# Kernel tuning notes

Hardware: AMD Instinct MI355X
Metric: run time of the kernel (lower is better)

The kernel has to match this reference:

```python
import jax, jax.numpy as jnp
import numpy as np

BATCH_SIZE = 2048
N_PARENTS = 256
N_FEATURES = 32
N_GLOBAL = 16
N_BRANCHES = 4
OFFSET = 262144  # nodes from levels before the parent level


def reshape_features(mtx, n_parents, batch_size, n_branches, n_features):
    # Redistribute [n_parents*batch, n_branches*n_features] -> [n_parents*n_branches*batch, n_features]
    # preserving node>event>branch ordering, exactly as the torch.jit.script helper.
    m = mtx.reshape(n_parents, batch_size, n_features * n_branches)
    m = jnp.swapaxes(m, 1, 2)
    m = m.reshape(n_parents * n_branches, n_features, batch_size)
    m = jnp.swapaxes(m, 1, 2)
    return m.reshape(n_parents * n_branches * batch_size, n_features)


def setup_inputs() -> dict:
    key = jax.random.key(0)
    k = jax.random.split(key, 5)
    n_rows = OFFSET + N_PARENTS * BATCH_SIZE
    x = jax.random.normal(k[0], (n_rows, N_FEATURES), dtype=jnp.float32)
    global_features = jax.random.normal(k[1], (BATCH_SIZE, N_GLOBAL), dtype=jnp.float32)
    # parent nodes occupy contiguous rows [OFFSET, OFFSET + n_parents*batch)
    parents_idxs = jnp.arange(N_PARENTS * BATCH_SIZE, dtype=jnp.int32) + OFFSET
    d_in = N_FEATURES + N_GLOBAL
    d_out = N_FEATURES * N_BRANCHES
    W1 = jax.random.normal(k[2], (d_in, d_out), dtype=jnp.float32) * 0.05
    b1 = jnp.zeros((d_out,), dtype=jnp.float32)
    W2 = jax.random.normal(k[3], (d_out, d_out), dtype=jnp.float32) * 0.05
    b2 = jnp.zeros((d_out,), dtype=jnp.float32)
    return {"x": x, "global_features": global_features, "parents_idxs": parents_idxs,
            "W1": W1, "b1": b1, "W2": W2, "b2": b2}


def reference(x, global_features, parents_idxs, W1, b1, W2, b2):
    # Gather parent node features and per-event global features
    parents_ftxs = x[parents_idxs]                                   # [P*B, F]
    parent_global = global_features[parents_idxs % BATCH_SIZE]      # [P*B, G]
    h = jnp.concatenate([parents_ftxs, parent_global], axis=-1)     # [P*B, F+G]
    # proj_nn: small MLP (Linear -> LeakyReLU -> Linear), torch LeakyReLU default slope 0.01
    h = jax.nn.leaky_relu(h @ W1 + b1, negative_slope=0.01)
    proj_ftx = h @ W2 + b2                                           # [P*B, BR*F]
    # residual: repeat_interleave each feature n_branches times along feature dim
    proj_ftx = proj_ftx + jnp.repeat(parents_ftxs, N_BRANCHES, axis=-1)
    children_ftxs = reshape_features(proj_ftx, N_PARENTS, BATCH_SIZE, N_BRANCHES, N_FEATURES)
    return jnp.concatenate([x, children_ftxs], axis=0)
```

## Files before the change

kernel.cpp:

```cpp
#include <hip/hip_runtime.h>

#define BATCH   2048
#define NPAR    256
#define NF      32
#define NG      16
#define NBR     4
#define OFS     262144
#define DOUT    128
#define NROWSX  (OFS + NPAR*BATCH)
#define MROWS   (NPAR*BATCH)
#define NTILES  (MROWS/16)
#define CHBASE  (NROWSX*NF)
#define NMLP    4096
#define NCOPY   2048

typedef short bf16x8 __attribute__((ext_vector_type(8)));
typedef float f32x4  __attribute__((ext_vector_type(4)));

#define WSOFF_W2F  1048576
#define WSOFF_W1F  (1048576 + 32768)

__device__ __forceinline__ unsigned short f2bf(float f){
  unsigned int u = __float_as_uint(f);
  u += 0x7FFFu + ((u >> 16) & 1u);
  return (unsigned short)(u >> 16);
}

__global__ void k_g1(const float* __restrict__ gf, const float* __restrict__ W1,
                     const float* __restrict__ b1, const float* __restrict__ W2,
                     char* __restrict__ ws){
  int bid = blockIdx.x, tid = threadIdx.x;
  if (bid < 1024){
    int idx = bid*256 + tid;
    int e = idx >> 7, j = idx & 127;
    float s = b1[j];
    const float* grow = gf + e*NG;
    const float* w = W1 + NF*DOUT + j;
    #pragma unroll
    for (int k = 0; k < NG; k++) s = fmaf(grow[k], w[k*DOUT], s);
    ((float*)ws)[idx] = s;
    return;
  }
  int t = (bid - 1024)*256 + tid;
  if (t < 2048){
    int f = t >> 6, l = t & 63;
    int kk = f >> 3, n = f & 7;
    int krow = 32*kk + 8*(l >> 4);
    int col  = 16*n + (l & 15);
    union { uint4 q; unsigned short u[8]; } w;
    #pragma unroll
    for (int e = 0; e < 8; e++) w.u[e] = f2bf(W2[(krow + e)*DOUT + col]);
    ((uint4*)(ws + WSOFF_W2F))[t] = w.q;
  } else {
    int q = t - 2048;
    int n = q >> 6, l = q & 63;
    int kb = 8*(l >> 4);
    int col = 16*n + (l & 15);
    union { uint4 v; unsigned short u[8]; } w;
    #pragma unroll
    for (int e = 0; e < 8; e++) w.u[e] = f2bf(W1[(kb + e)*DOUT + col]);
    ((uint4*)(ws + WSOFF_W1F))[q] = w.v;
  }
}

__global__ __launch_bounds__(512, 4) void k_main(
    const float* __restrict__ x, const int* __restrict__ pidx,
    const float* __restrict__ b2, const char* __restrict__ ws,
    float* __restrict__ out)
{
  __shared__ uint4 sB2[2048];
  __shared__ uint4 sW1[512];
  __shared__ uint4 sH1[2048];

  const int bid = blockIdx.x;
  const int tid = threadIdx.x;

  if (bid % 3 == 2){
    const int cid = bid / 3;
    const int n = NROWSX*NF/4;
    const float4* src4 = (const float4*)x;
    float4* dst4 = (float4*)out;
    for (int i = cid*512 + tid; i < n; i += NCOPY*512)
      dst4[i] = src4[i];
    return;
  }
  const int mid = (bid/3)*2 + (bid % 3);

  const uint4* W2f = (const uint4*)(ws + WSOFF_W2F);
  const uint4* W1f = (const uint4*)(ws + WSOFF_W1F);
  #pragma unroll
  for (int i = 0; i < 4; i++) sB2[i*512 + tid] = W2f[i*512 + tid];
  sW1[tid] = W1f[tid & 511];
  __syncthreads();

  const int lane = tid & 63;
  const int wv   = tid >> 6;
  const int r15  = lane & 15;
  const int g    = lane >> 4;
  const float* G1 = (const float*)ws;

  char* h1base = (char*)sH1 + wv*4096;
  const bf16x8* B2f = (const bf16x8*)sB2;
  const bf16x8* B1f = (const bf16x8*)sW1;

  const int tl   = mid*8 + wv;
  const int row0 = tl*16;

  const int idxA = pidx[row0 + r15];

  const float* ap = x + idxA*NF + 8*g;
  float4 a0 = *(const float4*)ap;
  float4 a1 = *(const float4*)(ap + 4);
  float xres[8];
  #pragma unroll
  for (int n = 0; n < 8; n++) xres[n] = x[idxA*NF + 4*n + g];

  union { bf16x8 v; unsigned short u[8]; } af;
  af.u[0]=f2bf(a0.x); af.u[1]=f2bf(a0.y); af.u[2]=f2bf(a0.z); af.u[3]=f2bf(a0.w);
  af.u[4]=f2bf(a1.x); af.u[5]=f2bf(a1.y); af.u[6]=f2bf(a1.z); af.u[7]=f2bf(a1.w);

  const int g1r = idxA & (BATCH-1);
  f32x4 acc1[8];
  #pragma unroll
  for (int n = 0; n < 8; n++)
    acc1[n] = *(const f32x4*)(G1 + g1r*DOUT + 16*n + 4*g);
  #pragma unroll
  for (int n = 0; n < 8; n++)
    acc1[n] = __builtin_amdgcn_mfma_f32_16x16x32_bf16(B1f[n*64 + lane], af.v, acc1[n], 0, 0, 0);

  #pragma unroll
  for (int n = 0; n < 8; n++){
    float v0 = acc1[n][0], v1 = acc1[n][1], v2 = acc1[n][2], v3 = acc1[n][3];
    v0 = v0 > 0.f ? v0 : 0.01f*v0;
    v1 = v1 > 0.f ? v1 : 0.01f*v1;
    v2 = v2 > 0.f ? v2 : 0.01f*v2;
    v3 = v3 > 0.f ? v3 : 0.01f*v3;
    uint2 pk;
    pk.x = (unsigned)f2bf(v0) | ((unsigned)f2bf(v1) << 16);
    pk.y = (unsigned)f2bf(v2) | ((unsigned)f2bf(v3) << 16);
    int off = r15*256 + (16*n + 4*g)*2;
    off ^= (r15 & 7) << 4;
    *(uint2*)(h1base + off) = pk;
  }

  f32x4 acc2[8];
  #pragma unroll
  for (int n = 0; n < 8; n++)
    acc2[n] = *(const f32x4*)(b2 + 16*n + 4*g);
  #pragma unroll
  for (int kk = 0; kk < 4; kk++){
    int roff = r15*256 + 64*kk + 16*g;
    roff ^= (r15 & 7) << 4;
    bf16x8 a2 = *(const bf16x8*)(h1base + roff);
    #pragma unroll
    for (int n = 0; n < 8; n++)
      acc2[n] = __builtin_amdgcn_mfma_f32_16x16x32_bf16(B2f[(kk*8 + n)*64 + lane], a2, acc2[n], 0, 0, 0);
  }

  const int p  = row0 >> 11;
  const int b0 = row0 & (BATCH-1);
  const int orow = CHBASE + ((p*NBR)*BATCH + b0 + r15)*NF;
  #pragma unroll
  for (int n = 0; n < 8; n++){
    int c0 = 16*n + 4*g;
    int br = c0 >> 5, fc0 = c0 & 31;
    f32x4 v = acc2[n];
    float rsd = xres[n];
    v[0] += rsd; v[1] += rsd; v[2] += rsd; v[3] += rsd;
    *(f32x4*)(out + orow + br*(BATCH*NF) + fc0) = v;
  }
}

extern "C" void kernel_launch(void* const* d_in, const int* in_sizes, int n_in,
                              void* d_out, int out_size, void* d_ws, size_t ws_size,
                              hipStream_t stream){
  const float* x   = (const float*)d_in[0];
  const float* gf  = (const float*)d_in[1];
  const int*   pidx= (const int*)d_in[2];
  const float* W1  = (const float*)d_in[3];
  const float* b1  = (const float*)d_in[4];
  const float* W2  = (const float*)d_in[5];
  const float* b2  = (const float*)d_in[6];
  float* out = (float*)d_out;
  char* ws   = (char*)d_ws;

  k_g1  <<<1034, 256, 0, stream>>>(gf, W1, b1, W2, ws);
  k_main<<<NMLP + NCOPY, 512, 0, stream>>>(x, pidx, b2, ws, out);
}
```

Before: 162.9 us.

## Fuse copy into MLP waves, process four tiles per wave with prefetch

```diff
diff --git a/kernel.cpp b/kernel.cpp
--- a/kernel.cpp
+++ b/kernel.cpp
@@ -1,4 +1,5 @@
 #include <hip/hip_runtime.h>
+#include <hip/hip_bf16.h>
 
 #define BATCH   2048
 #define NPAR    256
@@ -11,8 +12,8 @@
 #define MROWS   (NPAR*BATCH)
 #define NTILES  (MROWS/16)
 #define CHBASE  (NROWSX*NF)
-#define NMLP    4096
-#define NCOPY   2048
+#define NMLP    1024
+#define CPN4    (NROWSX*NF/4)
 
 typedef short bf16x8 __attribute__((ext_vector_type(8)));
 typedef float f32x4  __attribute__((ext_vector_type(4)));
@@ -75,22 +76,11 @@
   const int bid = blockIdx.x;
   const int tid = threadIdx.x;
 
-  if (bid % 3 == 2){
-    const int cid = bid / 3;
-    const int n = NROWSX*NF/4;
-    const float4* src4 = (const float4*)x;
-    float4* dst4 = (float4*)out;
-    for (int i = cid*512 + tid; i < n; i += NCOPY*512)
-      dst4[i] = src4[i];
-    return;
-  }
-  const int mid = (bid/3)*2 + (bid % 3);
-
   const uint4* W2f = (const uint4*)(ws + WSOFF_W2F);
   const uint4* W1f = (const uint4*)(ws + WSOFF_W1F);
   #pragma unroll
   for (int i = 0; i < 4; i++) sB2[i*512 + tid] = W2f[i*512 + tid];
-  sW1[tid] = W1f[tid & 511];
+  sW1[tid] = W1f[tid];
   __syncthreads();
 
   const int lane = tid & 63;
@@ -98,76 +88,117 @@
   const int r15  = lane & 15;
   const int g    = lane >> 4;
   const float* G1 = (const float*)ws;
+  const float4* src4 = (const float4*)x;
+  float4* dst4 = (float4*)out;
 
   char* h1base = (char*)sH1 + wv*4096;
   const bf16x8* B2f = (const bf16x8*)sB2;
   const bf16x8* B1f = (const bf16x8*)sW1;
 
-  const int tl   = mid*8 + wv;
-  const int row0 = tl*16;
-
-  const int idxA = pidx[row0 + r15];
-
-  const float* ap = x + idxA*NF + 8*g;
-  float4 a0 = *(const float4*)ap;
-  float4 a1 = *(const float4*)(ap + 4);
-  float xres[8];
+  const int w    = bid*8 + wv;
+  const int gtid = bid*512 + tid;
+
+  int idx4[4];
   #pragma unroll
-  for (int n = 0; n < 8; n++) xres[n] = x[idxA*NF + 4*n + g];
-
-  union { bf16x8 v; unsigned short u[8]; } af;
-  af.u[0]=f2bf(a0.x); af.u[1]=f2bf(a0.y); af.u[2]=f2bf(a0.z); af.u[3]=f2bf(a0.w);
-  af.u[4]=f2bf(a1.x); af.u[5]=f2bf(a1.y); af.u[6]=f2bf(a1.z); af.u[7]=f2bf(a1.w);
-
-  const int g1r = idxA & (BATCH-1);
-  f32x4 acc1[8];
+  for (int t = 0; t < 4; t++) idx4[t] = pidx[w*64 + t*16 + r15];
+
+  const float* ap0 = x + idx4[0]*NF + 8*g;
+  float4 a0 = *(const float4*)ap0;
+  float4 a1 = *(const float4*)(ap0 + 4);
+  f32x4 g1n[8];
+  {
+    const float* gp = G1 + (idx4[0] & (BATCH-1))*DOUT + 4*g;
+    #pragma unroll
+    for (int n = 0; n < 8; n++) g1n[n] = *(const f32x4*)(gp + 16*n);
+  }
+
   #pragma unroll
-  for (int n = 0; n < 8; n++)
-    acc1[n] = *(const f32x4*)(G1 + g1r*DOUT + 16*n + 4*g);
-  #pragma unroll
-  for (int n = 0; n < 8; n++)
-    acc1[n] = __builtin_amdgcn_mfma_f32_16x16x32_bf16(B1f[n*64 + lane], af.v, acc1[n], 0, 0, 0);
-
-  #pragma unroll
-  for (int n = 0; n < 8; n++){
-    float v0 = acc1[n][0], v1 = acc1[n][1], v2 = acc1[n][2], v3 = acc1[n][3];
-    v0 = v0 > 0.f ? v0 : 0.01f*v0;
-    v1 = v1 > 0.f ? v1 : 0.01f*v1;
-    v2 = v2 > 0.f ? v2 : 0.01f*v2;
-    v3 = v3 > 0.f ? v3 : 0.01f*v3;
-    uint2 pk;
-    pk.x = (unsigned)f2bf(v0) | ((unsigned)f2bf(v1) << 16);
-    pk.y = (unsigned)f2bf(v2) | ((unsigned)f2bf(v3) << 16);
-    int off = r15*256 + (16*n + 4*g)*2;
-    off ^= (r15 & 7) << 4;
-    *(uint2*)(h1base + off) = pk;
-  }
-
-  f32x4 acc2[8];
-  #pragma unroll
-  for (int n = 0; n < 8; n++)
-    acc2[n] = *(const f32x4*)(b2 + 16*n + 4*g);
-  #pragma unroll
-  for (int kk = 0; kk < 4; kk++){
-    int roff = r15*256 + 64*kk + 16*g;
-    roff ^= (r15 & 7) << 4;
-    bf16x8 a2 = *(const bf16x8*)(h1base + roff);
+  for (int t = 0; t < 4; t++){
+    const int row0 = w*64 + t*16;
+    const int idxA = idx4[t];
+
+    float4 cp0 = src4[(t*3+0)*(NMLP*512) + gtid];
+    float4 cp1 = src4[(t*3+1)*(NMLP*512) + gtid];
+    float4 cp2 = src4[(t*3+2)*(NMLP*512) + gtid];
+
+    union { bf16x8 v; __hip_bfloat162 h[4]; } af;
+    af.h[0] = __float22bfloat162_rn(make_float2(a0.x, a0.y));
+    af.h[1] = __float22bfloat162_rn(make_float2(a0.z, a0.w));
+    af.h[2] = __float22bfloat162_rn(make_float2(a1.x, a1.y));
+    af.h[3] = __float22bfloat162_rn(make_float2(a1.z, a1.w));
+
+    f32x4 acc1[8];
+    #pragma unroll
+    for (int n = 0; n < 8; n++) acc1[n] = g1n[n];
+
+    float4 a0n = a0, a1n = a1;
+    if (t < 3){
+      const float* apn = x + idx4[t+1]*NF + 8*g;
+      a0n = *(const float4*)apn;
+      a1n = *(const float4*)(apn + 4);
+    }
+
     #pragma unroll
     for (int n = 0; n < 8; n++)
-      acc2[n] = __builtin_amdgcn_mfma_f32_16x16x32_bf16(B2f[(kk*8 + n)*64 + lane], a2, acc2[n], 0, 0, 0);
-  }
-
-  const int p  = row0 >> 11;
-  const int b0 = row0 & (BATCH-1);
-  const int orow = CHBASE + ((p*NBR)*BATCH + b0 + r15)*NF;
-  #pragma unroll
-  for (int n = 0; n < 8; n++){
-    int c0 = 16*n + 4*g;
-    int br = c0 >> 5, fc0 = c0 & 31;
-    f32x4 v = acc2[n];
-    float rsd = xres[n];
-    v[0] += rsd; v[1] += rsd; v[2] += rsd; v[3] += rsd;
-    *(f32x4*)(out + orow + br*(BATCH*NF) + fc0) = v;
+      acc1[n] = __builtin_amdgcn_mfma_f32_16x16x32_bf16(B1f[n*64 + lane], af.v, acc1[n], 0, 0, 0);
+
+    #pragma unroll
+    for (int n = 0; n < 8; n++){
+      float v0 = acc1[n][0], v1 = acc1[n][1], v2 = acc1[n][2], v3 = acc1[n][3];
+      v0 = v0 > 0.f ? v0 : 0.01f*v0;
+      v1 = v1 > 0.f ? v1 : 0.01f*v1;
+      v2 = v2 > 0.f ? v2 : 0.01f*v2;
+      v3 = v3 > 0.f ? v3 : 0.01f*v3;
+      union { uint2 q; __hip_bfloat162 h[2]; } pk;
+      pk.h[0] = __float22bfloat162_rn(make_float2(v0, v1));
+      pk.h[1] = __float22bfloat162_rn(make_float2(v2, v3));
+      int off = r15*256 + (16*n + 4*g)*2;
+      off ^= (r15 & 7) << 4;
+      *(uint2*)(h1base + off) = pk.q;
+    }
+
+    if (t < 3){
+      const float* gp = G1 + (idx4[t+1] & (BATCH-1))*DOUT + 4*g;
+      #pragma unroll
+      for (int n = 0; n < 8; n++) g1n[n] = *(const f32x4*)(gp + 16*n);
+    }
+
+    float xres[8];
+    #pragma unroll
+    for (int n = 0; n < 8; n++) xres[n] = x[idxA*NF + 4*n + g];
+
+    f32x4 acc2[8];
+    #pragma unroll
+    for (int n = 0; n < 8; n++)
+      acc2[n] = *(const f32x4*)(b2 + 16*n + 4*g);
+    #pragma unroll
+    for (int kk = 0; kk < 4; kk++){
+      int roff = r15*256 + 64*kk + 16*g;
+      roff ^= (r15 & 7) << 4;
+      bf16x8 a2 = *(const bf16x8*)(h1base + roff);
+      #pragma unroll
+      for (int n = 0; n < 8; n++)
+        acc2[n] = __builtin_amdgcn_mfma_f32_16x16x32_bf16(B2f[(kk*8 + n)*64 + lane], a2, acc2[n], 0, 0, 0);
+    }
+
+    const int p  = row0 >> 11;
+    const int b0 = row0 & (BATCH-1);
+    const int orow = CHBASE + ((p*NBR)*BATCH + b0 + r15)*NF;
+    #pragma unroll
+    for (int n = 0; n < 8; n++){
+      int c0 = 16*n + 4*g;
+      int br = c0 >> 5, fc0 = c0 & 31;
+      f32x4 v = acc2[n];
+      float rsd = xres[n];
+      v[0] += rsd; v[1] += rsd; v[2] += rsd; v[3] += rsd;
+      *(f32x4*)(out + orow + br*(BATCH*NF) + fc0) = v;
+    }
+
+    dst4[(t*3+0)*(NMLP*512) + gtid] = cp0;
+    dst4[(t*3+1)*(NMLP*512) + gtid] = cp1;
+    dst4[(t*3+2)*(NMLP*512) + gtid] = cp2;
+
+    a0 = a0n; a1 = a1n;
   }
 }
 
@@ -185,5 +216,5 @@
   char* ws   = (char*)d_ws;
 
   k_g1  <<<1034, 256, 0, stream>>>(gf, W1, b1, W2, ws);
-  k_main<<<NMLP + NCOPY, 512, 0, stream>>>(x, pidx, b2, ws, out);
-}
+  k_main<<<NMLP, 512, 0, stream>>>(x, pidx, b2, ws, out);
+}
```

Measured after the change: 197.8 us. 21.4% more time.

## Loop four tiles per wave with prefetch and fold residual into MFMA

Applied to the files above, without the earlier changes.

```diff
diff --git a/kernel.cpp b/kernel.cpp
--- a/kernel.cpp
+++ b/kernel.cpp
@@ -1,4 +1,5 @@
 #include <hip/hip_runtime.h>
+#include <hip/hip_bf16.h>
 
 #define BATCH   2048
 #define NPAR    256
@@ -9,16 +10,17 @@
 #define DOUT    128
 #define NROWSX  (OFS + NPAR*BATCH)
 #define MROWS   (NPAR*BATCH)
-#define NTILES  (MROWS/16)
 #define CHBASE  (NROWSX*NF)
-#define NMLP    4096
+#define NMLP    1024
 #define NCOPY   2048
+#define CPN4    (NROWSX*NF/4)
 
 typedef short bf16x8 __attribute__((ext_vector_type(8)));
 typedef float f32x4  __attribute__((ext_vector_type(4)));
 
 #define WSOFF_W2F  1048576
 #define WSOFF_W1F  (1048576 + 32768)
+#define WSOFF_RF   (1048576 + 32768 + 8192)
 
 __device__ __forceinline__ unsigned short f2bf(float f){
   unsigned int u = __float_as_uint(f);
@@ -26,9 +28,9 @@
   return (unsigned short)(u >> 16);
 }
 
-__global__ void k_g1(const float* __restrict__ gf, const float* __restrict__ W1,
-                     const float* __restrict__ b1, const float* __restrict__ W2,
-                     char* __restrict__ ws){
+__global__ void k_prep(const float* __restrict__ gf, const float* __restrict__ W1,
+                       const float* __restrict__ b1, const float* __restrict__ W2,
+                       char* __restrict__ ws){
   int bid = blockIdx.x, tid = threadIdx.x;
   if (bid < 1024){
     int idx = bid*256 + tid;
@@ -51,7 +53,7 @@
     #pragma unroll
     for (int e = 0; e < 8; e++) w.u[e] = f2bf(W2[(krow + e)*DOUT + col]);
     ((uint4*)(ws + WSOFF_W2F))[t] = w.q;
-  } else {
+  } else if (t < 2560){
     int q = t - 2048;
     int n = q >> 6, l = q & 63;
     int kb = 8*(l >> 4);
@@ -60,6 +62,15 @@
     #pragma unroll
     for (int e = 0; e < 8; e++) w.u[e] = f2bf(W1[(kb + e)*DOUT + col]);
     ((uint4*)(ws + WSOFF_W1F))[q] = w.v;
+  } else {
+    int q = t - 2560;
+    int n = q >> 6, l = q & 63;
+    int g = l >> 4, r = l & 15;
+    int e1 = 4*n + (r >> 2) - 8*g;
+    union { uint4 v; unsigned short u[8]; } w;
+    #pragma unroll
+    for (int e = 0; e < 8; e++) w.u[e] = (e == e1) ? 0x3F80 : 0;
+    ((uint4*)(ws + WSOFF_RF))[q] = w.v;
   }
 }
 
@@ -69,28 +80,28 @@
     float* __restrict__ out)
 {
   __shared__ uint4 sB2[2048];
-  __shared__ uint4 sW1[512];
+  __shared__ uint4 sWR[1024];
   __shared__ uint4 sH1[2048];
 
   const int bid = blockIdx.x;
   const int tid = threadIdx.x;
 
-  if (bid % 3 == 2){
-    const int cid = bid / 3;
-    const int n = NROWSX*NF/4;
+  if (bid % 3){
+    const int cid = (bid/3)*2 + (bid % 3) - 1;
     const float4* src4 = (const float4*)x;
     float4* dst4 = (float4*)out;
-    for (int i = cid*512 + tid; i < n; i += NCOPY*512)
+    for (int i = cid*512 + tid; i < CPN4; i += NCOPY*512)
       dst4[i] = src4[i];
     return;
   }
-  const int mid = (bid/3)*2 + (bid % 3);
+  const int mid = bid/3;
 
   const uint4* W2f = (const uint4*)(ws + WSOFF_W2F);
-  const uint4* W1f = (const uint4*)(ws + WSOFF_W1F);
+  const uint4* WRf = (const uint4*)(ws + WSOFF_W1F);
   #pragma unroll
   for (int i = 0; i < 4; i++) sB2[i*512 + tid] = W2f[i*512 + tid];
-  sW1[tid] = W1f[tid & 511];
+  sWR[tid] = WRf[tid];
+  sWR[512 + tid] = WRf[512 + tid];
   __syncthreads();
 
   const int lane = tid & 63;
@@ -101,73 +112,85 @@
 
   char* h1base = (char*)sH1 + wv*4096;
   const bf16x8* B2f = (const bf16x8*)sB2;
-  const bf16x8* B1f = (const bf16x8*)sW1;
-
-  const int tl   = mid*8 + wv;
-  const int row0 = tl*16;
-
-  const int idxA = pidx[row0 + r15];
-
+  const bf16x8* B1f = (const bf16x8*)sWR;
+  const bf16x8* Rf  = (const bf16x8*)(sWR + 512);
+
+  const int w = mid*8 + wv;
+
+  int idxA = pidx[w*64 + r15];
   const float* ap = x + idxA*NF + 8*g;
   float4 a0 = *(const float4*)ap;
   float4 a1 = *(const float4*)(ap + 4);
-  float xres[8];
-  #pragma unroll
-  for (int n = 0; n < 8; n++) xres[n] = x[idxA*NF + 4*n + g];
-
-  union { bf16x8 v; unsigned short u[8]; } af;
-  af.u[0]=f2bf(a0.x); af.u[1]=f2bf(a0.y); af.u[2]=f2bf(a0.z); af.u[3]=f2bf(a0.w);
-  af.u[4]=f2bf(a1.x); af.u[5]=f2bf(a1.y); af.u[6]=f2bf(a1.z); af.u[7]=f2bf(a1.w);
-
-  const int g1r = idxA & (BATCH-1);
-  f32x4 acc1[8];
-  #pragma unroll
-  for (int n = 0; n < 8; n++)
-    acc1[n] = *(const f32x4*)(G1 + g1r*DOUT + 16*n + 4*g);
-  #pragma unroll
-  for (int n = 0; n < 8; n++)
-    acc1[n] = __builtin_amdgcn_mfma_f32_16x16x32_bf16(B1f[n*64 + lane], af.v, acc1[n], 0, 0, 0);
-
-  #pragma unroll
-  for (int n = 0; n < 8; n++){
-    float v0 = acc1[n][0], v1 = acc1[n][1], v2 = acc1[n][2], v3 = acc1[n][3];
-    v0 = v0 > 0.f ? v0 : 0.01f*v0;
-    v1 = v1 > 0.f ? v1 : 0.01f*v1;
-    v2 = v2 > 0.f ? v2 : 0.01f*v2;
-    v3 = v3 > 0.f ? v3 : 0.01f*v3;
-    uint2 pk;
-    pk.x = (unsigned)f2bf(v0) | ((unsigned)f2bf(v1) << 16);
-    pk.y = (unsigned)f2bf(v2) | ((unsigned)f2bf(v3) << 16);
-    int off = r15*256 + (16*n + 4*g)*2;
-    off ^= (r15 & 7) << 4;
-    *(uint2*)(h1base + off) = pk;
-  }
-
-  f32x4 acc2[8];
-  #pragma unroll
-  for (int n = 0; n < 8; n++)
-    acc2[n] = *(const f32x4*)(b2 + 16*n + 4*g);
-  #pragma unroll
-  for (int kk = 0; kk < 4; kk++){
-    int roff = r15*256 + 64*kk + 16*g;
-    roff ^= (r15 & 7) << 4;
-    bf16x8 a2 = *(const bf16x8*)(h1base + roff);
-    #pragma unroll
-    for (int n = 0; n < 8; n++)
-      acc2[n] = __builtin_amdgcn_mfma_f32_16x16x32_bf16(B2f[(kk*8 + n)*64 + lane], a2, acc2[n], 0, 0, 0);
-  }
-
-  const int p  = row0 >> 11;
-  const int b0 = row0 & (BATCH-1);
-  const int orow = CHBASE + ((p*NBR)*BATCH + b0 + r15)*NF;
-  #pragma unroll
-  for (int n = 0; n < 8; n++){
-    int c0 = 16*n + 4*g;
-    int br = c0 >> 5, fc0 = c0 & 31;
-    f32x4 v = acc2[n];
-    float rsd = xres[n];
-    v[0] += rsd; v[1] += rsd; v[2] += rsd; v[3] += rsd;
-    *(f32x4*)(out + orow + br*(BATCH*NF) + fc0) = v;
+
+  for (int t = 0; t < 4; t++){
+    const int row0 = w*64 + t*16;
+
+    const int tn = (t < 3) ? t+1 : 3;
+    const int idxn = pidx[w*64 + tn*16 + r15];
+
+    const int g1r = idxA & (BATCH-1);
+    f32x4 acc1[8];
+    #pragma unroll
+    for (int n = 0; n < 8; n++)
+      acc1[n] = *(const f32x4*)(G1 + g1r*DOUT + 16*n + 4*g);
+
+    union { bf16x8 v; __hip_bfloat162 h[4]; } af;
+    af.h[0] = __float22bfloat162_rn(make_float2(a0.x, a0.y));
+    af.h[1] = __float22bfloat162_rn(make_float2(a0.z, a0.w));
+    af.h[2] = __float22bfloat162_rn(make_float2(a1.x, a1.y));
+    af.h[3] = __float22bfloat162_rn(make_float2(a1.z, a1.w));
+
+    #pragma unroll
+    for (int n = 0; n < 8; n++)
+      acc1[n] = __builtin_amdgcn_mfma_f32_16x16x32_bf16(B1f[n*64 + lane], af.v, acc1[n], 0, 0, 0);
+
+    const float* apn = x + idxn*NF + 8*g;
+    float4 a0n = *(const float4*)apn;
+    float4 a1n = *(const float4*)(apn + 4);
+
+    #pragma unroll
+    for (int n = 0; n < 8; n++){
+      float v0 = acc1[n][0], v1 = acc1[n][1], v2 = acc1[n][2], v3 = acc1[n][3];
+      v0 = v0 > 0.f ? v0 : 0.01f*v0;
+      v1 = v1 > 0.f ? v1 : 0.01f*v1;
+      v2 = v2 > 0.f ? v2 : 0.01f*v2;
+      v3 = v3 > 0.f ? v3 : 0.01f*v3;
+      union { uint2 q; __hip_bfloat162 h[2]; } pk;
+      pk.h[0] = __float22bfloat162_rn(make_float2(v0, v1));
+      pk.h[1] = __float22bfloat162_rn(make_float2(v2, v3));
+      int off = r15*256 + (16*n + 4*g)*2;
+      off ^= (r15 & 7) << 4;
+      *(uint2*)(h1base + off) = pk.q;
+    }
+
+    f32x4 acc2[8];
+    #pragma unroll
+    for (int n = 0; n < 8; n++)
+      acc2[n] = *(const f32x4*)(b2 + 16*n + 4*g);
+    #pragma unroll
+    for (int n = 0; n < 8; n++)
+      acc2[n] = __builtin_amdgcn_mfma_f32_16x16x32_bf16(Rf[n*64 + lane], af.v, acc2[n], 0, 0, 0);
+    #pragma unroll
+    for (int kk = 0; kk < 4; kk++){
+      int roff = r15*256 + 64*kk + 16*g;
+      roff ^= (r15 & 7) << 4;
+      bf16x8 a2 = *(const bf16x8*)(h1base + roff);
+      #pragma unroll
+      for (int n = 0; n < 8; n++)
+        acc2[n] = __builtin_amdgcn_mfma_f32_16x16x32_bf16(B2f[(kk*8 + n)*64 + lane], a2, acc2[n], 0, 0, 0);
+    }
+
+    const int p  = row0 >> 11;
+    const int b0 = row0 & (BATCH-1);
+    const int orow = CHBASE + ((p*NBR)*BATCH + b0 + r15)*NF;
+    #pragma unroll
+    for (int n = 0; n < 8; n++){
+      int c0 = 16*n + 4*g;
+      int br = c0 >> 5, fc0 = c0 & 31;
+      *(f32x4*)(out + orow + br*(BATCH*NF) + fc0) = acc2[n];
+    }
+
+    idxA = idxn; a0 = a0n; a1 = a1n;
   }
 }
 
@@ -184,6 +207,6 @@
   float* out = (float*)d_out;
   char* ws   = (char*)d_ws;
 
-  k_g1  <<<1034, 256, 0, stream>>>(gf, W1, b1, W2, ws);
+  k_prep<<<1036, 256, 0, stream>>>(gf, W1, b1, W2, ws);
   k_main<<<NMLP + NCOPY, 512, 0, stream>>>(x, pidx, b2, ws, out);
 }
```

New measurement: 425.4 us. 161% more time.
